# Optimization experiments

Measured on AMD Instinct MI355X. Metric: run time of the kernel, lower is better.

The kernel has to match this reference:

```python
import jax, jax.numpy as jnp
import numpy as np

N = 8_000_000
LOG_HALF = -0.6931471805599453  # log(1/2)

DATASET_MAP = {0: 0, 1: 0, 2: 0, 3: 0, 4: 1, 5: 1, 6: 1, 7: 1}
LOSS_RECIPE = [(0, 4, 4), (0, 6, 4), (1, 5, 5), (1, 6, 5), (2, 4, 4), (2, 5, 5), (2, 6, 6), (2, 7, 7),
               (4, 0, 4), (4, 2, 4), (5, 1, 5), (5, 2, 5), (6, 2, 6), (7, 2, 7)]
NEG_LOSS_RECIPE = [(0, 4, 1), (0, 4, 2), (0, 6, 1), (0, 6, 2), (1, 5, 0), (1, 5, 2), (1, 6, 0), (1, 6, 2),
                   (2, 4, 1), (2, 4, 2), (2, 5, 0), (2, 5, 2), (4, 0, 1), (4, 0, 2), (4, 2, 1), (4, 2, 2),
                   (5, 1, 0), (5, 1, 2), (5, 2, 0), (5, 2, 2), (2, 7, 2), (7, 2, 2)]


def log1mexp(x):
    """Numerically stable log(1 - exp(x)) for x < 0 (grad-safe where)."""
    big = x > LOG_HALF
    xb = jnp.where(big, x, -1.0)   # branch-safe operands
    xs = jnp.where(big, -1.0, x)
    return jnp.where(big, jnp.log(-jnp.expm1(xb)), jnp.log1p(-jnp.exp(xs)))


def create_probabilities(v1, v2):
    l1, l2 = log1mexp(v1), log1mexp(v2)
    return [v1 + l2, l1 + v2, v1 + v2, l1 + l2]  # PC, CP, CR, NR


def setup_inputs() -> dict:
    key = jax.random.key(0)
    ks = jax.random.split(key, 9)
    def vol(k):
        u = jax.random.uniform(k, (N, 2), dtype=jnp.float32, minval=1e-6, maxval=1.0 - 1e-6)
        return jnp.log(u)  # strictly negative log-probabilities
    names = ["vol_AB", "vol_BA", "vol_BC", "vol_CB", "vol_AC", "vol_CA"]
    inp = {n: vol(k) for n, k in zip(names, ks[:6])}
    inp["xy_rel_id"] = jax.random.randint(ks[6], (N, 2), 0, 2)
    inp["yz_rel_id"] = jax.random.randint(ks[7], (N, 2), 0, 2)
    inp["xz_rel_id"] = jax.random.randint(ks[8], (N, 2), 0, 2)
    return inp


def reference(vol_AB, vol_BA, vol_BC, vol_CB, vol_AC, vol_CA, xy_rel_id, yz_rel_id, xz_rel_id):
    pAB = create_probabilities(vol_AB, vol_BA)
    pBC = create_probabilities(vol_BC, vol_CB)
    pAC = create_probabilities(vol_AC, vol_CA)
    loss = jnp.float32(0.0)
    for xy, yz, xz in LOSS_RECIPE:
        f1, f2, f3 = DATASET_MAP[xy], DATASET_MAP[yz], DATASET_MAP[xz]
        term = pAB[xy % 4][:, f1] + pBC[yz % 4][:, f2] - pAC[xz % 4][:, f3]
        loss = loss + jnp.maximum(0.0, term).sum()
    for xy, yz, xz in NEG_LOSS_RECIPE:
        f1, f2, f3 = DATASET_MAP[xy], DATASET_MAP[yz], DATASET_MAP[xz]
        term = pAB[xy % 4][:, f1] + pBC[yz % 4][:, f2] - log1mexp(pAC[xz % 4][:, f3])
        loss = loss + jnp.maximum(0.0, term).sum()
    return loss
```

## Files before the change

kernel.cpp:

```cpp
#include <hip/hip_runtime.h>


#define LOG2E 1.4426950408889634f
#define LN2   0.6931471805599453f

__device__ __forceinline__ float fexp2(float x) { return __builtin_amdgcn_exp2f(x); }
__device__ __forceinline__ float flog2(float x) { return __builtin_amdgcn_logf(x); }
__device__ __forceinline__ float relu_(float x) { return fmaxf(x, 0.0f); }

__device__ __forceinline__ float row_loss_l2(
    float a0, float a1, float b0, float b1,
    float c0, float c1, float d0, float d1,
    float e0, float e1, float f0, float f1)
{
    float a0s = a0 * LOG2E, a1s = a1 * LOG2E;
    float b0s = b0 * LOG2E, b1s = b1 * LOG2E;
    float c0s = c0 * LOG2E, c1s = c1 * LOG2E;
    float d0s = d0 * LOG2E, d1s = d1 * LOG2E;
    float e0s = e0 * LOG2E, e1s = e1 * LOG2E;
    float f0s = f0 * LOG2E, f1s = f1 * LOG2E;

    float ua0 = fexp2(a0s), ub0 = fexp2(b0s), uc0 = fexp2(c0s), ud0 = fexp2(d0s);
    float ue0 = fexp2(e0s), uf0 = fexp2(f0s);
    float ua1 = fexp2(a1s), ub1 = fexp2(b1s), uc1 = fexp2(c1s), ud1 = fexp2(d1s);
    float ue1 = fexp2(e1s), uf1 = fexp2(f1s);

    float wa0 = 1.0f - ua0, wb0 = 1.0f - ub0, wc0 = 1.0f - uc0, wd0 = 1.0f - ud0;
    float we0 = 1.0f - ue0, wf0 = 1.0f - uf0;
    float wa1 = 1.0f - ua1, wb1 = 1.0f - ub1, wc1 = 1.0f - uc1, wd1 = 1.0f - ud1;
    float we1 = 1.0f - ue1, wf1 = 1.0f - uf1;

    float la0 = flog2(wa0), lb0 = flog2(wb0), lc0 = flog2(wc0), ld0 = flog2(wd0);
    float la1 = flog2(wa1), lb1 = flog2(wb1), lc1 = flog2(wc1), ld1 = flog2(wd1);
    float le1 = flog2(we1), lf1 = flog2(wf1);

    float LAC0 = flog2(fmaf(-ue0, wf0, 1.0f));
    float LAC1 = flog2(fmaf(-we0, uf0, 1.0f));
    float LAC2 = flog2(fmaf(-ue0, uf0, 1.0f));

    float AB00 = a0s + lb0, AB10 = la0 + b0s, AB20 = a0s + b0s;
    float AB01 = a1s + lb1, AB11 = la1 + b1s, AB21 = a1s + b1s, AB31 = la1 + lb1;
    float BC00 = c0s + ld0, BC10 = lc0 + d0s, BC20 = c0s + d0s;
    float BC01 = c1s + ld1, BC11 = lc1 + d1s, BC21 = c1s + d1s, BC31 = lc1 + ld1;
    float AC01 = e1s + lf1, AC11 = le1 + f1s, AC21 = e1s + f1s, AC31 = le1 + lf1;

    float s1  = AB00 + BC01, s2  = AB00 + BC21, s3  = AB10 + BC11, s4  = AB10 + BC21;
    float s5  = AB20 + BC01, s6  = AB20 + BC11, s7  = AB20 + BC21, s8  = AB20 + BC31;
    float s9  = AB01 + BC00, s10 = AB01 + BC20, s11 = AB11 + BC10, s12 = AB11 + BC20;
    float s13 = AB21 + BC20, s14 = AB31 + BC20;

    float p = 0.0f, q = 0.0f;
    p += relu_(s1 - AC01) + relu_(s2 - AC01) + relu_(s3 - AC11) + relu_(s4 - AC11);
    q += relu_(s5 - AC01) + relu_(s6 - AC11) + relu_(s7 - AC21) + relu_(s8 - AC31);
    p += relu_(s9 - AC01) + relu_(s10 - AC01) + relu_(s11 - AC11) + relu_(s12 - AC11);
    q += relu_(s13 - AC21) + relu_(s14 - AC31);
    p += relu_(s1 - LAC1) + relu_(s1 - LAC2) + relu_(s2 - LAC1) + relu_(s2 - LAC2);
    q += relu_(s3 - LAC0) + relu_(s3 - LAC2) + relu_(s4 - LAC0) + relu_(s4 - LAC2);
    p += relu_(s5 - LAC1) + relu_(s5 - LAC2) + relu_(s6 - LAC0) + relu_(s6 - LAC2);
    q += relu_(s9 - LAC1) + relu_(s9 - LAC2) + relu_(s10 - LAC1) + relu_(s10 - LAC2);
    p += relu_(s11 - LAC0) + relu_(s11 - LAC2) + relu_(s12 - LAC0) + relu_(s12 - LAC2);
    q += relu_(s8 - LAC2) + relu_(s14 - LAC2);
    return p + q;
}

struct Seg {
    float4 ab, ba, bc, cb, ac, ca;
};

__device__ __forceinline__ float pair_loss(const Seg& s)
{
    return row_loss_l2(s.ab.x, s.ab.y, s.ba.x, s.ba.y, s.bc.x, s.bc.y,
                       s.cb.x, s.cb.y, s.ac.x, s.ac.y, s.ca.x, s.ca.y)
         + row_loss_l2(s.ab.z, s.ab.w, s.ba.z, s.ba.w, s.bc.z, s.bc.w,
                       s.cb.z, s.cb.w, s.ac.z, s.ac.w, s.ca.z, s.ca.w);
}

__global__ __launch_bounds__(256)
__attribute__((amdgpu_waves_per_eu(2, 5)))
void box_loss_kernel(
    const float* __restrict__ AB, const float* __restrict__ BA,
    const float* __restrict__ BC, const float* __restrict__ CB,
    const float* __restrict__ AC, const float* __restrict__ CA,
    float* __restrict__ out, unsigned nElems)
{
    const unsigned nE = nElems;
    const unsigned T = (unsigned)gridDim.x * blockDim.x * 4u;
    unsigned t = ((unsigned)blockIdx.x * blockDim.x + threadIdx.x) * 4u;

    const unsigned nT = (nE + T - 1u) / T;
    const int pairs = (int)((nT + 1u) / 2u);

    #define LOAD_SEG(dst, msk, base)                        \
        do {                                                \
            bool v_ = ((base) + 4u) <= nE;                  \
            unsigned a_ = v_ ? (base) : 0u;                 \
            (msk) = v_ ? 1.0f : 0.0f;                       \
            (dst).ab = *(const float4*)(AB + a_);           \
            (dst).ba = *(const float4*)(BA + a_);           \
            (dst).bc = *(const float4*)(BC + a_);           \
            (dst).cb = *(const float4*)(CB + a_);           \
            (dst).ac = *(const float4*)(AC + a_);           \
            (dst).ca = *(const float4*)(CA + a_);           \
        } while (0)

    Seg X, Y;
    float mX, mY;

    LOAD_SEG(X, mX, t); t += T;
    LOAD_SEG(Y, mY, t); t += T;
    __builtin_amdgcn_sched_barrier(0);

    float acc = 0.0f;
    for (int r = 0; r < pairs - 1; ++r) {
        acc += mX * pair_loss(X);
        LOAD_SEG(X, mX, t); t += T;
        __builtin_amdgcn_sched_barrier(0);

        acc += mY * pair_loss(Y);
        LOAD_SEG(Y, mY, t); t += T;
        __builtin_amdgcn_sched_barrier(0);
    }
    acc += mX * pair_loss(X);
    acc += mY * pair_loss(Y);
    #undef LOAD_SEG

    acc *= LN2;

    #pragma unroll
    for (int off = 32; off > 0; off >>= 1)
        acc += __shfl_down(acc, off, 64);

    __shared__ float wsum[4];
    const int lane = threadIdx.x & 63;
    const int wid  = threadIdx.x >> 6;
    if (lane == 0) wsum[wid] = acc;
    __syncthreads();
    if (threadIdx.x == 0) {
        float s = wsum[0] + wsum[1] + wsum[2] + wsum[3];
        atomicAdd(out, s);
    }
}

extern "C" void kernel_launch(void* const* d_in, const int* in_sizes, int n_in,
                              void* d_out, int out_size, void* d_ws, size_t ws_size,
                              hipStream_t stream) {
    const float* AB = (const float*)d_in[0];
    const float* BA = (const float*)d_in[1];
    const float* BC = (const float*)d_in[2];
    const float* CB = (const float*)d_in[3];
    const float* AC = (const float*)d_in[4];
    const float* CA = (const float*)d_in[5];

    const unsigned nElems = (unsigned)in_sizes[0];
    const int block = 256;
    const int grid = 2560;

    hipMemsetAsync(d_out, 0, (size_t)out_size * sizeof(float), stream);
    box_loss_kernel<<<grid, block, 0, stream>>>(AB, BA, BC, CB, AC, CA,
                                                (float*)d_out, nElems);
}
```

Before: 440.3 us.

## Shrink per-thread work to one row per segment and raise occupancy target

Each thread now loads float2 (one row) per input instead of float4 (two rows), which halves live registers per segment. The waves-per-EU hint goes from 2-5 to 6-8 and the grid drops from 2560 to 2048 blocks. The aim is more waves in flight to hide memory latency. The cost is narrower loads and more loop iterations per element.

```diff
diff --git a/kernel.cpp b/kernel.cpp
--- a/kernel.cpp
+++ b/kernel.cpp
@@ -63,20 +63,18 @@
     return p + q;
 }
 
-struct Seg {
-    float4 ab, ba, bc, cb, ac, ca;
+struct Seg2 {
+    float2 ab, ba, bc, cb, ac, ca;
 };
 
-__device__ __forceinline__ float pair_loss(const Seg& s)
+__device__ __forceinline__ float row_loss_seg(const Seg2& s)
 {
     return row_loss_l2(s.ab.x, s.ab.y, s.ba.x, s.ba.y, s.bc.x, s.bc.y,
-                       s.cb.x, s.cb.y, s.ac.x, s.ac.y, s.ca.x, s.ca.y)
-         + row_loss_l2(s.ab.z, s.ab.w, s.ba.z, s.ba.w, s.bc.z, s.bc.w,
-                       s.cb.z, s.cb.w, s.ac.z, s.ac.w, s.ca.z, s.ca.w);
+                       s.cb.x, s.cb.y, s.ac.x, s.ac.y, s.ca.x, s.ca.y);
 }
 
 __global__ __launch_bounds__(256)
-__attribute__((amdgpu_waves_per_eu(2, 5)))
+__attribute__((amdgpu_waves_per_eu(6, 8)))
 void box_loss_kernel(
     const float* __restrict__ AB, const float* __restrict__ BA,
     const float* __restrict__ BC, const float* __restrict__ CB,
@@ -84,26 +82,26 @@
     float* __restrict__ out, unsigned nElems)
 {
     const unsigned nE = nElems;
-    const unsigned T = (unsigned)gridDim.x * blockDim.x * 4u;
-    unsigned t = ((unsigned)blockIdx.x * blockDim.x + threadIdx.x) * 4u;
+    const unsigned T = (unsigned)gridDim.x * blockDim.x * 2u;
+    unsigned t = ((unsigned)blockIdx.x * blockDim.x + threadIdx.x) * 2u;
 
     const unsigned nT = (nE + T - 1u) / T;
     const int pairs = (int)((nT + 1u) / 2u);
 
     #define LOAD_SEG(dst, msk, base)                        \
         do {                                                \
-            bool v_ = ((base) + 4u) <= nE;                  \
+            bool v_ = ((base) + 2u) <= nE;                  \
             unsigned a_ = v_ ? (base) : 0u;                 \
             (msk) = v_ ? 1.0f : 0.0f;                       \
-            (dst).ab = *(const float4*)(AB + a_);           \
-            (dst).ba = *(const float4*)(BA + a_);           \
-            (dst).bc = *(const float4*)(BC + a_);           \
-            (dst).cb = *(const float4*)(CB + a_);           \
-            (dst).ac = *(const float4*)(AC + a_);           \
-            (dst).ca = *(const float4*)(CA + a_);           \
+            (dst).ab = *(const float2*)(AB + a_);           \
+            (dst).ba = *(const float2*)(BA + a_);           \
+            (dst).bc = *(const float2*)(BC + a_);           \
+            (dst).cb = *(const float2*)(CB + a_);           \
+            (dst).ac = *(const float2*)(AC + a_);           \
+            (dst).ca = *(const float2*)(CA + a_);           \
         } while (0)
 
-    Seg X, Y;
+    Seg2 X, Y;
     float mX, mY;
 
     LOAD_SEG(X, mX, t); t += T;
@@ -112,16 +110,16 @@
 
     float acc = 0.0f;
     for (int r = 0; r < pairs - 1; ++r) {
-        acc += mX * pair_loss(X);
+        acc += mX * row_loss_seg(X);
         LOAD_SEG(X, mX, t); t += T;
         __builtin_amdgcn_sched_barrier(0);
 
-        acc += mY * pair_loss(Y);
+        acc += mY * row_loss_seg(Y);
         LOAD_SEG(Y, mY, t); t += T;
         __builtin_amdgcn_sched_barrier(0);
     }
-    acc += mX * pair_loss(X);
-    acc += mY * pair_loss(Y);
+    acc += mX * row_loss_seg(X);
+    acc += mY * row_loss_seg(Y);
     #undef LOAD_SEG
 
     acc *= LN2;
@@ -153,7 +151,7 @@
 
     const unsigned nElems = (unsigned)in_sizes[0];
     const int block = 256;
-    const int grid = 2560;
+    const int grid = 2048;
 
     hipMemsetAsync(d_out, 0, (size_t)out_size * sizeof(float), stream);
     box_loss_kernel<<<grid, block, 0, stream>>>(AB, BA, BC, CB, AC, CA,
```

New measurement: 512.5 us. +16.4%, slower.
